# Kernel tuning notes

Hardware: AMD Instinct MI355X
Metric: run time of the kernel (lower is better)

## Reference

```python
import jax, jax.numpy as jnp
import numpy as np

N = 100000
E = 1600000
D = 128          # in_feat == hidden_size
L = 3            # hidden layers
EPS = 1e-5       # BatchNorm1d eps


def setup_inputs() -> dict:
    key = jax.random.key(0)
    ks = jax.random.split(key, 12)
    x = jax.random.normal(ks[0], (N, D), dtype=jnp.float32)
    edge_index = jax.random.randint(ks[1], (2, E), 0, N, dtype=jnp.int64)
    s = 1.0 / np.sqrt(D)
    # stacked hidden-layer SAGEConv params: lin_l (neighbor), lin_r (root), bias on lin_l
    Wl = jax.random.uniform(ks[2], (L, D, D), jnp.float32, -s, s)
    Wr = jax.random.uniform(ks[3], (L, D, D), jnp.float32, -s, s)
    b = jax.random.uniform(ks[4], (L, D), jnp.float32, -s, s)
    # batchnorm affine params
    gamma = jnp.ones((L, D), jnp.float32)
    beta = jnp.zeros((L, D), jnp.float32)
    # output SAGEConv: D -> 1
    Wl_out = jax.random.uniform(ks[5], (D, 1), jnp.float32, -s, s)
    Wr_out = jax.random.uniform(ks[6], (D, 1), jnp.float32, -s, s)
    b_out = jax.random.uniform(ks[7], (1,), jnp.float32, -s, s)
    return {"x": x, "edge_index": edge_index, "Wl": Wl, "Wr": Wr, "b": b,
            "gamma": gamma, "beta": beta, "Wl_out": Wl_out, "Wr_out": Wr_out,
            "b_out": b_out}


def _sage(x, src, dst, inv_deg, Wl, Wr, b):
    # gather neighbor features along edges, mean-aggregate at destination
    msg_sum = jax.ops.segment_sum(x[src], dst, num_segments=N)   # [N, F]
    mean = msg_sum * inv_deg                                     # 0 for isolated nodes
    return mean @ Wl + x @ Wr + b


def _batchnorm(x, gamma, beta):
    m = jnp.mean(x, axis=0)
    v = jnp.mean((x - m) ** 2, axis=0)  # biased var, as torch BN uses for normalization
    return gamma * (x - m) * jax.lax.rsqrt(v + EPS) + beta


def reference(x, edge_index, Wl, Wr, b, gamma, beta, Wl_out, Wr_out, b_out):
    src, dst = edge_index[0], edge_index[1]
    deg = jax.ops.segment_sum(jnp.ones((E,), x.dtype), dst, num_segments=N)
    inv_deg = jnp.where(deg > 0, 1.0 / jnp.maximum(deg, 1.0), 0.0)[:, None]
    h = x
    for i in range(L):
        h = _sage(h, src, dst, inv_deg, Wl[i], Wr[i], b[i])
        h = jax.nn.relu(h)
        h = _batchnorm(h, gamma[i], beta[i])
    out = _sage(h, src, dst, inv_deg, Wl_out, Wr_out, b_out)
    return jax.nn.sigmoid(out)  # [N, 1]
```

## Files before the change

### kernel.cpp

```cpp
#include <hip/hip_runtime.h>

typedef unsigned short u16;
typedef unsigned int u32;
typedef unsigned long long u64;

#define GN 100000
#define GE 1600000
#define DCAP 64
#define NRANGE 196
#define NBKT (NRANGE * 8)
#define BCAP 1536
#define LDA 136
#define CPSETS 64

typedef __bf16 bf16x8 __attribute__((ext_vector_type(8)));
typedef float f32x4 __attribute__((ext_vector_type(4)));
typedef float f32x2 __attribute__((ext_vector_type(2)));
typedef u32 u32x4 __attribute__((ext_vector_type(4)));
typedef u32 u32x2 __attribute__((ext_vector_type(2)));

__device__ __forceinline__ float bl(u32 u){ return __uint_as_float(u << 16); }
__device__ __forceinline__ float bh(u32 u){ return __uint_as_float(u & 0xffff0000u); }
__device__ __forceinline__ float bfu(u16 v){ return __uint_as_float(((u32)v) << 16); }
__device__ __forceinline__ u16 f2bf(float f){
    u32 u = __float_as_uint(f);
    u32 r = (u + 0x7fffu + ((u >> 16) & 1u)) >> 16;
    return (u16)r;
}
__device__ __forceinline__ u32 pack2(float a, float b){
    return (u32)f2bf(a) | ((u32)f2bf(b) << 16);
}
__device__ __forceinline__ u32 pk8x4(float a, float b, float c, float d){
    u32 p = (u32)__builtin_amdgcn_cvt_pk_fp8_f32(a, b, 0, false);
    p = (u32)__builtin_amdgcn_cvt_pk_fp8_f32(c, d, p, true);
    return p;
}

__global__ void __launch_bounds__(256) k_init(const int* ei, const u32* xraw,
                                              int* cursor, float* colpart, int* flags,
                                              int* bcur){
    int i = blockIdx.x * 256 + threadIdx.x;
    if (i < GN) cursor[i] = 0;
    if (i < NBKT) bcur[i] = 0;
    if (i < 3 * CPSETS * 256) colpart[i] = 0.f;
    int t = threadIdx.x;
    if (blockIdx.x == 0){
        __shared__ int s_any[4];
        int v = 0;
        #pragma unroll
        for (int j = 0; j < 4; ++j){
            int k = t * 4 + j;
            v |= ei[2 * k * 1000 + 1];
        }
        #pragma unroll
        for (int m = 1; m < 64; m <<= 1) v |= __shfl_xor(v, m);
        if ((t & 63) == 0) s_any[t >> 6] = v;
        __syncthreads();
        if (t == 0){
            int any = s_any[0] | s_any[1] | s_any[2] | s_any[3];
            flags[0] = (any == 0) ? 1 : 0;
        }
    }
    if (blockIdx.x == 1){
        __shared__ int s_cnt[4];
        int cnt = 0;
        #pragma unroll
        for (int j = 0; j < 4; ++j){
            int idx = (t * 4 + j) * 6000 + 3;
            u32 u = xraw[idx];
            int e = (u >> 7) & 0xFF;
            cnt += (e >= 100 && e <= 140) ? 1 : 0;
        }
        #pragma unroll
        for (int m = 1; m < 64; m <<= 1) cnt += __shfl_xor(cnt, m);
        if ((t & 63) == 0) s_cnt[t >> 6] = cnt;
        __syncthreads();
        if (t == 0){
            int tot = s_cnt[0] + s_cnt[1] + s_cnt[2] + s_cnt[3];
            flags[1] = (tot > 512) ? 0 : 1;
        }
    }
}

__global__ void __launch_bounds__(256) k_convx(const void* x, const int* flags,
                                               u16* xb, u32* h8){
    int tid = blockIdx.x * 256 + threadIdx.x;
    int node = tid >> 4, l15 = tid & 15;
    if (node >= GN) return;
    float f[8];
    if (flags[1]){
        const float* xf = (const float*)x + node * 128 + l15;
        #pragma unroll
        for (int a = 0; a < 8; ++a) f[a] = __builtin_nontemporal_load(xf + a * 16);
    } else {
        const u16* xh = (const u16*)x + node * 128 + l15;
        #pragma unroll
        for (int a = 0; a < 8; ++a) f[a] = bfu(xh[a * 16]);
    }
    u16* xo = xb + node * 128 + l15;
    #pragma unroll
    for (int a = 0; a < 8; ++a) xo[a * 16] = f2bf(f[a]);
    u32x2 e = { pk8x4(f[0], f[1], f[2], f[3]), pk8x4(f[4], f[5], f[6], f[7]) };
    ((u32x2*)h8)[node * 16 + l15] = e;
}

#define WOFF_WR    49152
#define WOFF_B     98304
#define WOFF_G     98688
#define WOFF_BE    99072
#define WOFF_WLO   99456
#define WOFF_WRO   99584
#define WOFF_BO    99712
#define WTOT       99713
__global__ void __launch_bounds__(256) k_convw(const void* Wl, const void* Wr, const void* b,
                                               const void* g, const void* be, const void* wlo,
                                               const void* wro, const void* bo,
                                               const int* flags, u16* wbuf, float* biasf){
    int i = blockIdx.x * 256 + threadIdx.x;
    if (i >= WTOT) return;
    const void* s; int k;
    if (i < WOFF_B){
        bool isWl = (i < WOFF_WR);
        const void* src = isWl ? Wl : Wr;
        int r = isWl ? i : i - WOFF_WR;
        int layer = r >> 14, L = r & 16383;
        int kk = isWl ? (((L & 7) << 4) | (L >> 10))
                      : (((L >> 10) << 3) | (L & 7));
        int cc = (L >> 3) & 127;
        int si = layer * 16384 + kk * 128 + cc;
        float fv = flags[1] ? ((const float*)src)[si] : bfu(((const u16*)src)[si]);
        wbuf[i] = f2bf(fv);
        return;
    }
    if      (i < WOFF_G  ){ s = b;   k = i - WOFF_B; }
    else if (i < WOFF_BE ){ s = g;   k = i - WOFF_G; }
    else if (i < WOFF_WLO){ s = be;  k = i - WOFF_BE; }
    else if (i < WOFF_WRO){ s = wlo; k = i - WOFF_WLO; }
    else if (i < WOFF_BO ){ s = wro; k = i - WOFF_WRO; }
    else                  { s = bo;  k = 0; }
    float fv = flags[1] ? ((const float*)s)[k] : bfu(((const u16*)s)[k]);
    wbuf[i] = f2bf(fv);
    if (i >= WOFF_B && i < WOFF_B + 384) biasf[i - WOFF_B] = fv;
}

__global__ void __launch_bounds__(256) k_fillA(const int* ei, const int* flags,
                                               int* bcur, u64* pairs){
    __shared__ int cnt[256];
    __shared__ int lofs[256];
    __shared__ int gbase[NRANGE];
    __shared__ int wsum[4];
    __shared__ u64 lp[1024];
    int t = threadIdx.x;
    int lane = t & 63, w = t >> 6;
    int res = blockIdx.x & 7;
    int base = blockIdx.x * 1024;
    int is64 = flags[0];
    cnt[t] = 0;
    __syncthreads();
    int myd[4], mys[4], slot[4], myr[4];
    #pragma unroll
    for (int j = 0; j < 4; ++j){
        int e = base + j * 256 + t;
        if (e < GE){
            int d, s;
            if (is64){ d = __builtin_nontemporal_load(ei + 2 * (GE + e));
                       s = __builtin_nontemporal_load(ei + 2 * e); }
            else     { d = __builtin_nontemporal_load(ei + GE + e);
                       s = __builtin_nontemporal_load(ei + e); }
            myd[j] = d; mys[j] = s; myr[j] = d >> 9;
            slot[j] = atomicAdd(&cnt[myr[j]], 1);
        } else myr[j] = -1;
    }
    __syncthreads();
    int v = cnt[t];
    int sv = v;
    #pragma unroll
    for (int d = 1; d < 64; d <<= 1){
        int u = __shfl_up(sv, d);
        if (lane >= d) sv += u;
    }
    if (lane == 63) wsum[w] = sv;
    __syncthreads();
    int prefix = 0;
    #pragma unroll
    for (int j = 0; j < 4; ++j) if (j < w) prefix += wsum[j];
    lofs[t] = sv + prefix - v;
    if (t < NRANGE && cnt[t] > 0)
        gbase[t] = atomicAdd(&bcur[t * 8 + res], cnt[t]);
    __syncthreads();
    #pragma unroll
    for (int j = 0; j < 4; ++j){
        if (myr[j] >= 0)
            lp[lofs[myr[j]] + slot[j]] = ((u64)(u32)myd[j] << 32) | (u32)mys[j];
    }
    __syncthreads();
    int total = GE - base; if (total > 1024) total = 1024;
    for (int i = t; i < total; i += 256){
        u64 pr = lp[i];
        int r = (int)(pr >> 32) >> 9;
        int g = gbase[r] + (i - lofs[r]);
        if (g < BCAP) pairs[((size_t)(r * 8 + res)) * BCAP + g] = pr;
    }
}

__global__ void __launch_bounds__(256) k_fillB(const int* bcur, const u64* pairs,
                                               int* cursor, int* col){
    int range = blockIdx.x % 200;
    int sub   = blockIdx.x / 200;
    if (range >= NRANGE || sub >= 8) return;
    int bkt = range * 8 + sub;
    int n = bcur[bkt]; if (n > BCAP) n = BCAP;
    const u64* P = pairs + (size_t)bkt * BCAP;
    for (int i = threadIdx.x; i < n; i += 256){
        u64 pr = __builtin_nontemporal_load(P + i);
        int s = (int)(u32)pr, d = (int)(pr >> 32);
        int pos = atomicAdd(&cursor[d], 1);
        if (pos < DCAP) col[d * DCAP + pos] = s;
    }
}

__global__ void __launch_bounds__(128, 6) k_gemm(const u32* h8, const int* deg, const int* col,
                                                 const u16* hin,
                                                 const u16* Wlp, const u16* Wrp,
                                                 const float* biasf, u16* hout,
                                                 u32* h8o, int write8, float* colpart){
    __shared__ u16 smA[32 * LDA];
    int t = threadIdx.x;
    int wid = t >> 6, lane = t & 63;
    int quad = lane >> 4, l15 = lane & 15;
    int r0 = blockIdx.x * 32;
    int wr0 = wid * 16;

    {
        int g8 = lane >> 3, lg8 = lane & 7;
        const u32x4* hrow4 = (const u32x4*)h8;
        #define ACC16(v) { \
            a01 += __builtin_amdgcn_cvt_pk_f32_fp8((v).x, false); \
            a23 += __builtin_amdgcn_cvt_pk_f32_fp8((v).x, true);  \
            a45 += __builtin_amdgcn_cvt_pk_f32_fp8((v).y, false); \
            a67 += __builtin_amdgcn_cvt_pk_f32_fp8((v).y, true);  \
            b01 += __builtin_amdgcn_cvt_pk_f32_fp8((v).z, false); \
            b23 += __builtin_amdgcn_cvt_pk_f32_fp8((v).z, true);  \
            b45 += __builtin_amdgcn_cvt_pk_f32_fp8((v).w, false); \
            b67 += __builtin_amdgcn_cvt_pk_f32_fp8((v).w, true); }
        #pragma unroll
        for (int m = 0; m < 2; ++m){
            int lr = wr0 + (g8 << 1) + m;
            int node = r0 + lr;
            f32x2 a01 = {0.f,0.f}, a23 = {0.f,0.f}, a45 = {0.f,0.f}, a67 = {0.f,0.f};
            f32x2 b01 = {0.f,0.f}, b23 = {0.f,0.f}, b45 = {0.f,0.f}, b67 = {0.f,0.f};
            int d = 0;
            if (node < GN){
                d = deg[node];
                int cnt = d < DCAP ? d : DCAP;
                const int* nb = col + node * DCAP;
                int e = 0;
                for (; e + 7 < cnt; e += 8){
                    int4 n0 = *(const int4*)(nb + e);
                    int4 n1 = *(const int4*)(nb + e + 4);
                    u32x4 v0 = hrow4[(size_t)n0.x * 8 + lg8];
                    u32x4 v1 = hrow4[(size_t)n0.y * 8 + lg8];
                    u32x4 v2 = hrow4[(size_t)n0.z * 8 + lg8];
                    u32x4 v3 = hrow4[(size_t)n0.w * 8 + lg8];
                    u32x4 v4 = hrow4[(size_t)n1.x * 8 + lg8];
                    u32x4 v5 = hrow4[(size_t)n1.y * 8 + lg8];
                    u32x4 v6 = hrow4[(size_t)n1.z * 8 + lg8];
                    u32x4 v7 = hrow4[(size_t)n1.w * 8 + lg8];
                    ACC16(v0) ACC16(v1) ACC16(v2) ACC16(v3)
                    ACC16(v4) ACC16(v5) ACC16(v6) ACC16(v7)
                }
                for (; e + 1 < cnt; e += 2){
                    u32x4 v0 = hrow4[(size_t)nb[e]     * 8 + lg8];
                    u32x4 v1 = hrow4[(size_t)nb[e + 1] * 8 + lg8];
                    ACC16(v0) ACC16(v1)
                }
                if (e < cnt){
                    u32x4 v0 = hrow4[(size_t)nb[e] * 8 + lg8];
                    ACC16(v0)
                }
            }
            float inv = (d > 0) ? 1.f / (float)d : 0.f;
            f32x2 iv = {inv, inv};
            a01 *= iv; a23 *= iv; a45 *= iv; a67 *= iv;
            b01 *= iv; b23 *= iv; b45 *= iv; b67 *= iv;
            u32x4 o0, o1;
            o0.x = pack2(a01.x, a01.y); o0.y = pack2(a23.x, a23.y);
            o0.z = pack2(a45.x, a45.y); o0.w = pack2(a67.x, a67.y);
            o1.x = pack2(b01.x, b01.y); o1.y = pack2(b23.x, b23.y);
            o1.z = pack2(b45.x, b45.y); o1.w = pack2(b67.x, b67.y);
            u16* wp = smA + lr * LDA + (lg8 << 4);
            *(u32x4*)wp = o0;
            *(u32x4*)(wp + 8) = o1;
        }
        #undef ACC16
    }
    __asm__ volatile("s_waitcnt lgkmcnt(0)" ::: "memory");
    __builtin_amdgcn_sched_barrier(0);

    f32x4 acc[8];
    #pragma unroll
    for (int j = 0; j < 8; j++) acc[j] = (f32x4){0.f, 0.f, 0.f, 0.f};

    int node0 = r0 + wr0 + l15;

    {
        const u32x4* Wg = (const u32x4*)Wlp;
        const u16* a0 = smA + (wr0 + l15) * LDA;
        #pragma unroll
        for (int s = 0; s < 4; ++s){
            int kc = (s << 2) + quad;
            union { u32x4 u; bf16x8 v; } fa0;
            fa0.u = *(const u32x4*)(a0 + (kc << 3));
            const u32x4* wg = Wg + (kc << 7) + l15;
            #pragma unroll
            for (int cb = 0; cb < 8; ++cb){
                union { u32x4 u; bf16x8 v; } fw;
                fw.u = wg[cb << 4];
                acc[cb] = __builtin_amdgcn_mfma_f32_16x16x32_bf16(fa0.v, fw.v, acc[cb], 0, 0, 0);
            }
        }
    }
    {
        const u32x4* Wg = (const u32x4*)Wrp;
        #pragma unroll
        for (int s = 0; s < 4; ++s){
            int kk = (s << 5) + (quad << 3);
            union { u32x4 u; bf16x8 v; } fa0;
            fa0.u = (node0 < GN) ? *(const u32x4*)(hin + node0 * 128 + kk) : (u32x4){0,0,0,0};
            int kc = (s << 2) + quad;
            const u32x4* wg = Wg + (kc << 7) + l15;
            #pragma unroll
            for (int cb = 0; cb < 8; ++cb){
                union { u32x4 u; bf16x8 v; } fw;
                fw.u = wg[cb << 4];
                acc[cb] = __builtin_amdgcn_mfma_f32_16x16x32_bf16(fa0.v, fw.v, acc[cb], 0, 0, 0);
            }
        }
    }

    float bsv[8];
    #pragma unroll
    for (int cb = 0; cb < 8; cb++) bsv[cb] = biasf[cb * 16 + l15];
    float csum[8], csq[8];
    #pragma unroll
    for (int cb = 0; cb < 8; cb++){ csum[cb] = 0.f; csq[cb] = 0.f; }

    #pragma unroll
    for (int rr = 0; rr < 4; ++rr){
        int row = r0 + wr0 + quad * 4 + rr;
        float v[8];
        #pragma unroll
        for (int cb = 0; cb < 8; ++cb) v[cb] = fmaxf(acc[cb][rr] + bsv[cb], 0.f);
        if (row < GN){
            #pragma unroll
            for (int cb = 0; cb < 8; ++cb){
                hout[row * 128 + cb * 16 + l15] = f2bf(v[cb]);
                csum[cb] += v[cb]; csq[cb] += v[cb] * v[cb];
            }
            if (write8){
                u32x2 pp = { pk8x4(v[0], v[1], v[2], v[3]),
                             pk8x4(v[4], v[5], v[6], v[7]) };
                ((u32x2*)h8o)[row * 16 + l15] = pp;
            }
        }
    }
    int base = (blockIdx.x & (CPSETS - 1)) * 256;
    #pragma unroll
    for (int cb = 0; cb < 8; cb++){
        float cs = csum[cb], cq = csq[cb];
        cs += __shfl_xor(cs, 16); cs += __shfl_xor(cs, 32);
        cq += __shfl_xor(cq, 16); cq += __shfl_xor(cq, 32);
        if (quad == 0){
            atomicAdd(&colpart[base + cb * 16 + l15], cs);
            atomicAdd(&colpart[base + 128 + cb * 16 + l15], cq);
        }
    }
}

__global__ void __launch_bounds__(256) k_bnf(const float* colpart, const u16* gamma, const u16* beta,
                                             int mode,
                                             const u16* WlN, const u16* WrN, u16* wfd,
                                             const float* bNsrc, float* bNdst,
                                             const u16* wlo, const u16* wro, const u16* bo,
                                             u16* hwl, u16* hwr, float* hb){
    __shared__ float s_sc[128], s_sh[128], s_red[256];
    int t = threadIdx.x, b = blockIdx.x;
    if (t < 128){
        float s = 0.f, q = 0.f;
        for (int j = 0; j < CPSETS; ++j){
            s += colpart[j * 256 + t];
            q += colpart[j * 256 + 128 + t];
        }
        const float invn = 1.f / (float)GN;
        float mean = s * invn;
        float var = fmaxf(q * invn - mean * mean, 0.f);
        float rstd = rsqrtf(var + 1e-5f);
        float g  = bfu(gamma[t]);
        float be = bfu(beta[t]);
        float sc = g * rstd, sh = be - mean * sc;
        s_sc[t] = sc; s_sh[t] = sh;
    }
    __syncthreads();
    if (mode == 0){
        if (b < 64){
            int idx = b * 256 + t;
            int kl = ((idx & 7) << 4) | (idx >> 10);
            int kr = ((idx >> 10) << 3) | (idx & 7);
            wfd[idx]         = f2bf(s_sc[kl] * bfu(WlN[idx]));
            wfd[16384 + idx] = f2bf(s_sc[kr] * bfu(WrN[idx]));
        } else if (t < 128){
            float acc = bNsrc[t];
            for (int k = 0; k < 128; ++k){
                int Ll = ((k & 15) << 10) + (t << 3) + (k >> 4);
                int Lr = ((k >> 3) << 10) + (t << 3) + (k & 7);
                acc += s_sh[k] * (bfu(WlN[Ll]) + bfu(WrN[Lr]));
            }
            bNdst[t] = acc;
        }
    } else if (b == 64){
        float contrib = 0.f;
        if (t < 128){
            float wl = bfu(wlo[t]), wr = bfu(wro[t]);
            hwl[t] = f2bf(s_sc[t] * wl);
            hwr[t] = f2bf(s_sc[t] * wr);
            contrib = s_sh[t] * (wl + wr);
        }
        s_red[t] = contrib;
        __syncthreads();
        for (int off = 128; off >= 1; off >>= 1){
            if (t < off) s_red[t] += s_red[t + off];
            __syncthreads();
        }
        if (t == 0) hb[0] = s_red[0] + bfu(bo[0]);
    }
}

__global__ void __launch_bounds__(256) k_dot(const u16* h, const u16* wl, const u16* wr,
                                             float* y, float* r){
    int node = (blockIdx.x * 256 + threadIdx.x) >> 6;
    int lane = threadIdx.x & 63;
    if (node >= GN) return;
    u32 hv  = ((const u32*)h)[node * 64 + lane];
    u32 wlv = ((const u32*)wl)[lane];
    u32 wrv = ((const u32*)wr)[lane];
    float hlo = bl(hv), hhi = bh(hv);
    float ya = hlo * bl(wlv) + hhi * bh(wlv);
    float ra = hlo * bl(wrv) + hhi * bh(wrv);
    #pragma unroll
    for (int m = 1; m < 64; m <<= 1){ ya += __shfl_xor(ya, m); ra += __shfl_xor(ra, m); }
    if (lane == 0){ y[node] = ya; r[node] = ra; }
}

__global__ void __launch_bounds__(64) k_out(const float* y, const float* r, const int* deg,
                                            const int* col, const float* hb,
                                            const int* flags, void* out){
    int lane = threadIdx.x;
    int grp = lane >> 4, lg = lane & 15;
    int node = blockIdx.x * 4 + grp;
    if (node >= GN) return;
    int d = deg[node];
    int cnt = d < DCAP ? d : DCAP;
    const int* nb = col + node * DCAP;
    float s = 0.f;
    for (int e = lg; e < cnt; e += 16) s += y[nb[e]];
    s += __shfl_xor(s, 1); s += __shfl_xor(s, 2);
    s += __shfl_xor(s, 4); s += __shfl_xor(s, 8);
    if (lg == 0){
        float inv = (d > 0) ? 1.f / (float)d : 0.f;
        float z = inv * s + r[node] + hb[0];
        float sg = 1.f / (1.f + __expf(-z));
        if (flags[1]) ((float*)out)[node] = sg;
        else          ((u16*)out)[node] = f2bf(sg);
    }
}

extern "C" void kernel_launch(void* const* d_in, const int* in_sizes, int n_in,
                              void* d_out, int out_size, void* d_ws, size_t ws_size,
                              hipStream_t stream) {
    const void* x     = d_in[0];
    const int*  ei    = (const int*)d_in[1];
    const void* Wl    = d_in[2];
    const void* Wr    = d_in[3];
    const void* bias  = d_in[4];
    const void* gamma = d_in[5];
    const void* beta  = d_in[6];
    const void* wlout = d_in[7];
    const void* wrout = d_in[8];
    const void* bout  = d_in[9];

    char* p = (char*)d_ws;
    auto take = [&](size_t b){ void* q = (void*)p; p += (b + 255) & ~(size_t)255; return q; };
    int*   cursor = (int*)  take((size_t)GN * 4);
    int*   flags  = (int*)  take(256);
    int*   bcur   = (int*)  take((size_t)NBKT * 4);
    float* colpart= (float*)take((size_t)3 * CPSETS * 256 * 4);
    float* biasf  = (float*)take(384 * 4);
    float* bf2    = (float*)take(128 * 4);
    float* bf3    = (float*)take(128 * 4);
    float* hb     = (float*)take(256);
    u16*   wf2    = (u16*)  take(32768 * 2);
    u16*   wf3    = (u16*)  take(32768 * 2);
    u16*   hwl    = (u16*)  take(128 * 2);
    u16*   hwr    = (u16*)  take(128 * 2);
    float* yv     = (float*)take((size_t)GN * 4);
    float* rv     = (float*)take((size_t)GN * 4);
    int*   col    = (int*)  take((size_t)GN * DCAP * 4);
    u16*   xb     = (u16*)  take((size_t)GN * 128 * 2);
    u16*   hbuf   = (u16*)  take((size_t)GN * 128 * 2);
    u32*   h8a    = (u32*)  take((size_t)GN * 128);
    u32*   h8b    = (u32*)  take((size_t)GN * 128);
    u64*   pairs  = (u64*)  take((size_t)NBKT * BCAP * 8);
    u16*   wbuf   = (u16*)  take((size_t)WTOT * 2);

    const int NB_N = (GN + 255) / 256;
    const int NB_W = (GN + 3) / 4;
    const int NB_G = (GN + 31) / 32;
    const int NB_M = (GN * 16 + 255) / 256;
    const int NB_C = (WTOT + 255) / 256;
    const int NB_A = (GE + 1023) / 1024;
    const int NB_O = (GN + 3) / 4;

    k_init <<<NB_N, 256, 0, stream>>>(ei, (const u32*)x, cursor, colpart, flags, bcur);
    k_convx<<<NB_M, 256, 0, stream>>>(x, flags, xb, h8a);
    k_convw<<<NB_C, 256, 0, stream>>>(Wl, Wr, bias, gamma, beta, wlout, wrout, bout, flags, wbuf, biasf);
    k_fillA<<<NB_A, 256, 0, stream>>>(ei, flags, bcur, pairs);
    k_fillB<<<1600, 256, 0, stream>>>(bcur, pairs, cursor, col);

    const u16* hin = xb;
    for (int i = 0; i < 3; ++i){
        const u16* Wlp; const u16* Wrp; const float* bfi;
        if (i == 0){ Wlp = wbuf;     Wrp = wbuf + WOFF_WR; bfi = biasf; }
        else if (i == 1){ Wlp = wf2; Wrp = wf2 + 16384;    bfi = bf2; }
        else { Wlp = wf3;            Wrp = wf3 + 16384;    bfi = bf3; }
        u16* wfd = (i == 0) ? wf2 : wf3;
        float* bNdst = (i == 0) ? bf2 : bf3;
        int nx = (i < 2) ? (i + 1) : 0;
        const u32* h8i = (i == 1) ? h8b : h8a;
        u32*       h8o = (i == 0) ? h8b : h8a;
        k_gemm<<<NB_G, 128, 0, stream>>>(h8i, cursor, col, hin, Wlp, Wrp, bfi,
                                         hbuf, (i == 2) ? h8b : h8o, (i < 2) ? 1 : 0,
                                         colpart + i * CPSETS * 256);
        k_bnf <<<65, 256, 0, stream>>>(colpart + i * CPSETS * 256,
            wbuf + WOFF_G + i * 128, wbuf + WOFF_BE + i * 128, (i == 2) ? 1 : 0,
            wbuf + nx * 16384, wbuf + WOFF_WR + nx * 16384, wfd,
            biasf + nx * 128, bNdst,
            wbuf + WOFF_WLO, wbuf + WOFF_WRO, wbuf + WOFF_BO, hwl, hwr, hb);
        hin = hbuf;
    }
    k_dot<<<NB_W, 256, 0, stream>>>(hbuf, hwl, hwr, yv, rv);
    k_out<<<NB_O, 64, 0, stream>>>(yv, rv, cursor, col, hb, flags, d_out);
}
```

Baseline: 433.3 us.

## Build CSR per range with shared-memory atomics and interleave two-node neighbor gathers

k_fillB now runs one block per 512-node range. It counts degrees with LDS atomics, writes the cursor directly, then scatters column indices using LDS cursors instead of global atomics. This removes global atomic traffic, but each range is now handled by a single block, which lowers parallelism. The k_gemm gather gives each lane 8 bytes of a row, so 16 lanes cover one row. Each loop iteration fetches neighbors of two nodes together to get more loads in flight, and launch bounds drop to 5 waves to leave room for the extra registers.

New measurement: 469.8 us. +8.4%, slower.

```diff
diff --git a/kernel.cpp b/kernel.cpp
--- a/kernel.cpp
+++ b/kernel.cpp
@@ -205,21 +205,46 @@
 
 __global__ void __launch_bounds__(256) k_fillB(const int* bcur, const u64* pairs,
                                                int* cursor, int* col){
-    int range = blockIdx.x % 200;
-    int sub   = blockIdx.x / 200;
-    if (range >= NRANGE || sub >= 8) return;
-    int bkt = range * 8 + sub;
-    int n = bcur[bkt]; if (n > BCAP) n = BCAP;
-    const u64* P = pairs + (size_t)bkt * BCAP;
-    for (int i = threadIdx.x; i < n; i += 256){
-        u64 pr = __builtin_nontemporal_load(P + i);
-        int s = (int)(u32)pr, d = (int)(pr >> 32);
-        int pos = atomicAdd(&cursor[d], 1);
-        if (pos < DCAP) col[d * DCAP + pos] = s;
-    }
-}
-
-__global__ void __launch_bounds__(128, 6) k_gemm(const u32* h8, const int* deg, const int* col,
+    __shared__ int cnt[512];
+    int r = blockIdx.x;
+    int t = threadIdx.x;
+    cnt[t] = 0; cnt[t + 256] = 0;
+    __syncthreads();
+    int base = r * 512;
+    int nsb[8];
+    #pragma unroll
+    for (int sb = 0; sb < 8; ++sb){
+        int n = bcur[r * 8 + sb];
+        nsb[sb] = n < BCAP ? n : BCAP;
+    }
+    #pragma unroll
+    for (int sb = 0; sb < 8; ++sb){
+        const u64* P = pairs + (size_t)(r * 8 + sb) * BCAP;
+        for (int i = t; i < nsb[sb]; i += 256){
+            int d = (int)(P[i] >> 32);
+            atomicAdd(&cnt[d - base], 1);
+        }
+    }
+    __syncthreads();
+    int n0 = base + t, n1 = base + t + 256;
+    if (n0 < GN) cursor[n0] = cnt[t];
+    if (n1 < GN) cursor[n1] = cnt[t + 256];
+    __syncthreads();
+    cnt[t] = 0; cnt[t + 256] = 0;
+    __syncthreads();
+    #pragma unroll
+    for (int sb = 0; sb < 8; ++sb){
+        const u64* P = pairs + (size_t)(r * 8 + sb) * BCAP;
+        for (int i = t; i < nsb[sb]; i += 256){
+            u64 pr = P[i];
+            int s = (int)(u32)pr, d = (int)(pr >> 32) - base;
+            int pos = atomicAdd(&cnt[d], 1);
+            if (pos < DCAP) col[(base + d) * DCAP + pos] = s;
+        }
+    }
+}
+
+__global__ void __launch_bounds__(128, 5) k_gemm(const u32* h8, const int* deg, const int* col,
                                                  const u16* hin,
                                                  const u16* Wlp, const u16* Wrp,
                                                  const float* biasf, u16* hout,
@@ -232,67 +257,90 @@
     int wr0 = wid * 16;
 
     {
-        int g8 = lane >> 3, lg8 = lane & 7;
-        const u32x4* hrow4 = (const u32x4*)h8;
-        #define ACC16(v) { \
-            a01 += __builtin_amdgcn_cvt_pk_f32_fp8((v).x, false); \
-            a23 += __builtin_amdgcn_cvt_pk_f32_fp8((v).x, true);  \
-            a45 += __builtin_amdgcn_cvt_pk_f32_fp8((v).y, false); \
-            a67 += __builtin_amdgcn_cvt_pk_f32_fp8((v).y, true);  \
-            b01 += __builtin_amdgcn_cvt_pk_f32_fp8((v).z, false); \
-            b23 += __builtin_amdgcn_cvt_pk_f32_fp8((v).z, true);  \
-            b45 += __builtin_amdgcn_cvt_pk_f32_fp8((v).w, false); \
-            b67 += __builtin_amdgcn_cvt_pk_f32_fp8((v).w, true); }
-        #pragma unroll
-        for (int m = 0; m < 2; ++m){
-            int lr = wr0 + (g8 << 1) + m;
-            int node = r0 + lr;
-            f32x2 a01 = {0.f,0.f}, a23 = {0.f,0.f}, a45 = {0.f,0.f}, a67 = {0.f,0.f};
-            f32x2 b01 = {0.f,0.f}, b23 = {0.f,0.f}, b45 = {0.f,0.f}, b67 = {0.f,0.f};
-            int d = 0;
-            if (node < GN){
-                d = deg[node];
-                int cnt = d < DCAP ? d : DCAP;
-                const int* nb = col + node * DCAP;
-                int e = 0;
-                for (; e + 7 < cnt; e += 8){
-                    int4 n0 = *(const int4*)(nb + e);
-                    int4 n1 = *(const int4*)(nb + e + 4);
-                    u32x4 v0 = hrow4[(size_t)n0.x * 8 + lg8];
-                    u32x4 v1 = hrow4[(size_t)n0.y * 8 + lg8];
-                    u32x4 v2 = hrow4[(size_t)n0.z * 8 + lg8];
-                    u32x4 v3 = hrow4[(size_t)n0.w * 8 + lg8];
-                    u32x4 v4 = hrow4[(size_t)n1.x * 8 + lg8];
-                    u32x4 v5 = hrow4[(size_t)n1.y * 8 + lg8];
-                    u32x4 v6 = hrow4[(size_t)n1.z * 8 + lg8];
-                    u32x4 v7 = hrow4[(size_t)n1.w * 8 + lg8];
-                    ACC16(v0) ACC16(v1) ACC16(v2) ACC16(v3)
-                    ACC16(v4) ACC16(v5) ACC16(v6) ACC16(v7)
-                }
-                for (; e + 1 < cnt; e += 2){
-                    u32x4 v0 = hrow4[(size_t)nb[e]     * 8 + lg8];
-                    u32x4 v1 = hrow4[(size_t)nb[e + 1] * 8 + lg8];
-                    ACC16(v0) ACC16(v1)
-                }
-                if (e < cnt){
-                    u32x4 v0 = hrow4[(size_t)nb[e] * 8 + lg8];
-                    ACC16(v0)
-                }
-            }
-            float inv = (d > 0) ? 1.f / (float)d : 0.f;
-            f32x2 iv = {inv, inv};
-            a01 *= iv; a23 *= iv; a45 *= iv; a67 *= iv;
-            b01 *= iv; b23 *= iv; b45 *= iv; b67 *= iv;
-            u32x4 o0, o1;
-            o0.x = pack2(a01.x, a01.y); o0.y = pack2(a23.x, a23.y);
-            o0.z = pack2(a45.x, a45.y); o0.w = pack2(a67.x, a67.y);
-            o1.x = pack2(b01.x, b01.y); o1.y = pack2(b23.x, b23.y);
-            o1.z = pack2(b45.x, b45.y); o1.w = pack2(b67.x, b67.y);
-            u16* wp = smA + lr * LDA + (lg8 << 4);
-            *(u32x4*)wp = o0;
-            *(u32x4*)(wp + 8) = o1;
-        }
-        #undef ACC16
+        int g16 = lane >> 4, lg = lane & 15;
+        const u32x2* hrow2 = (const u32x2*)h8;
+        #define ACC8(v, P0, P1, P2, P3) { \
+            P0 += __builtin_amdgcn_cvt_pk_f32_fp8((v).x, false); \
+            P1 += __builtin_amdgcn_cvt_pk_f32_fp8((v).x, true);  \
+            P2 += __builtin_amdgcn_cvt_pk_f32_fp8((v).y, false); \
+            P3 += __builtin_amdgcn_cvt_pk_f32_fp8((v).y, true); }
+        #pragma unroll
+        for (int pm = 0; pm < 2; ++pm){
+            int lrA = wr0 + (g16 << 2) + (pm << 1);
+            int lrB = lrA + 1;
+            int nA = r0 + lrA, nB = r0 + lrB;
+            int dA = (nA < GN) ? deg[nA] : 0;
+            int dB = (nB < GN) ? deg[nB] : 0;
+            int cA = dA < DCAP ? dA : DCAP;
+            int cB = dB < DCAP ? dB : DCAP;
+            const int* nbA = col + nA * DCAP;
+            const int* nbB = col + nB * DCAP;
+            f32x2 A0={0.f,0.f},A1={0.f,0.f},A2={0.f,0.f},A3={0.f,0.f};
+            f32x2 B0={0.f,0.f},B1={0.f,0.f},B2={0.f,0.f},B3={0.f,0.f};
+            int eA = 0, eB = 0;
+            while (eA + 7 < cA && eB + 7 < cB){
+                int4 iA0 = *(const int4*)(nbA + eA);
+                int4 iA1 = *(const int4*)(nbA + eA + 4);
+                int4 iB0 = *(const int4*)(nbB + eB);
+                int4 iB1 = *(const int4*)(nbB + eB + 4);
+                u32x2 a0 = hrow2[(size_t)iA0.x * 16 + lg];
+                u32x2 a1 = hrow2[(size_t)iA0.y * 16 + lg];
+                u32x2 a2 = hrow2[(size_t)iA0.z * 16 + lg];
+                u32x2 a3 = hrow2[(size_t)iA0.w * 16 + lg];
+                u32x2 a4 = hrow2[(size_t)iA1.x * 16 + lg];
+                u32x2 a5 = hrow2[(size_t)iA1.y * 16 + lg];
+                u32x2 a6 = hrow2[(size_t)iA1.z * 16 + lg];
+                u32x2 a7 = hrow2[(size_t)iA1.w * 16 + lg];
+                u32x2 b0 = hrow2[(size_t)iB0.x * 16 + lg];
+                u32x2 b1 = hrow2[(size_t)iB0.y * 16 + lg];
+                u32x2 b2 = hrow2[(size_t)iB0.z * 16 + lg];
+                u32x2 b3 = hrow2[(size_t)iB0.w * 16 + lg];
+                u32x2 b4 = hrow2[(size_t)iB1.x * 16 + lg];
+                u32x2 b5 = hrow2[(size_t)iB1.y * 16 + lg];
+                u32x2 b6 = hrow2[(size_t)iB1.z * 16 + lg];
+                u32x2 b7 = hrow2[(size_t)iB1.w * 16 + lg];
+                ACC8(a0,A0,A1,A2,A3) ACC8(a1,A0,A1,A2,A3)
+                ACC8(a2,A0,A1,A2,A3) ACC8(a3,A0,A1,A2,A3)
+                ACC8(a4,A0,A1,A2,A3) ACC8(a5,A0,A1,A2,A3)
+                ACC8(a6,A0,A1,A2,A3) ACC8(a7,A0,A1,A2,A3)
+                ACC8(b0,B0,B1,B2,B3) ACC8(b1,B0,B1,B2,B3)
+                ACC8(b2,B0,B1,B2,B3) ACC8(b3,B0,B1,B2,B3)
+                ACC8(b4,B0,B1,B2,B3) ACC8(b5,B0,B1,B2,B3)
+                ACC8(b6,B0,B1,B2,B3) ACC8(b7,B0,B1,B2,B3)
+                eA += 8; eB += 8;
+            }
+            for (; eA + 1 < cA; eA += 2){
+                u32x2 a0 = hrow2[(size_t)nbA[eA]     * 16 + lg];
+                u32x2 a1 = hrow2[(size_t)nbA[eA + 1] * 16 + lg];
+                ACC8(a0,A0,A1,A2,A3) ACC8(a1,A0,A1,A2,A3)
+            }
+            if (eA < cA){
+                u32x2 a0 = hrow2[(size_t)nbA[eA] * 16 + lg];
+                ACC8(a0,A0,A1,A2,A3)
+            }
+            for (; eB + 1 < cB; eB += 2){
+                u32x2 b0 = hrow2[(size_t)nbB[eB]     * 16 + lg];
+                u32x2 b1 = hrow2[(size_t)nbB[eB + 1] * 16 + lg];
+                ACC8(b0,B0,B1,B2,B3) ACC8(b1,B0,B1,B2,B3)
+            }
+            if (eB < cB){
+                u32x2 b0 = hrow2[(size_t)nbB[eB] * 16 + lg];
+                ACC8(b0,B0,B1,B2,B3)
+            }
+            float invA = (dA > 0) ? 1.f / (float)dA : 0.f;
+            float invB = (dB > 0) ? 1.f / (float)dB : 0.f;
+            f32x2 ivA = {invA, invA}, ivB = {invB, invB};
+            A0 *= ivA; A1 *= ivA; A2 *= ivA; A3 *= ivA;
+            B0 *= ivB; B1 *= ivB; B2 *= ivB; B3 *= ivB;
+            u32x4 oA, oB;
+            oA.x = pack2(A0.x, A0.y); oA.y = pack2(A1.x, A1.y);
+            oA.z = pack2(A2.x, A2.y); oA.w = pack2(A3.x, A3.y);
+            oB.x = pack2(B0.x, B0.y); oB.y = pack2(B1.x, B1.y);
+            oB.z = pack2(B2.x, B2.y); oB.w = pack2(B3.x, B3.y);
+            *(u32x4*)(smA + lrA * LDA + (lg << 3)) = oA;
+            *(u32x4*)(smA + lrB * LDA + (lg << 3)) = oB;
+        }
+        #undef ACC8
     }
     __asm__ volatile("s_waitcnt lgkmcnt(0)" ::: "memory");
     __builtin_amdgcn_sched_barrier(0);
@@ -524,7 +572,7 @@
     k_convx<<<NB_M, 256, 0, stream>>>(x, flags, xb, h8a);
     k_convw<<<NB_C, 256, 0, stream>>>(Wl, Wr, bias, gamma, beta, wlout, wrout, bout, flags, wbuf, biasf);
     k_fillA<<<NB_A, 256, 0, stream>>>(ei, flags, bcur, pairs);
-    k_fillB<<<1600, 256, 0, stream>>>(bcur, pairs, cursor, col);
+    k_fillB<<<NRANGE, 256, 0, stream>>>(bcur, pairs, cursor, col);
 
     const u16* hin = xb;
     for (int i = 0; i < 3; ++i){
```

## Build CSR columns per node range using shared-memory atomics in fillB

Applied to the files above, without the earlier changes.

The CSR fill kernel now launches one block per 512-node range instead of one per bucket. Each block first counts in-degrees with shared-memory atomics, writes them to the cursor array, then does a second pass that assigns slots with shared atomics. This replaces global atomics on the cursor array, which cuts global atomic traffic. In exchange it launches far fewer blocks (196 vs 1600), reads each range's pairs twice, and relies on cursor being written here rather than accumulated.

Result: faster. 423.0 us, median of 2 (-2.4%).

```diff
diff --git a/kernel.cpp b/kernel.cpp
--- a/kernel.cpp
+++ b/kernel.cpp
@@ -205,17 +205,42 @@
 
 __global__ void __launch_bounds__(256) k_fillB(const int* bcur, const u64* pairs,
                                                int* cursor, int* col){
-    int range = blockIdx.x % 200;
-    int sub   = blockIdx.x / 200;
-    if (range >= NRANGE || sub >= 8) return;
-    int bkt = range * 8 + sub;
-    int n = bcur[bkt]; if (n > BCAP) n = BCAP;
-    const u64* P = pairs + (size_t)bkt * BCAP;
-    for (int i = threadIdx.x; i < n; i += 256){
-        u64 pr = __builtin_nontemporal_load(P + i);
-        int s = (int)(u32)pr, d = (int)(pr >> 32);
-        int pos = atomicAdd(&cursor[d], 1);
-        if (pos < DCAP) col[d * DCAP + pos] = s;
+    __shared__ int cnt[512];
+    int r = blockIdx.x;
+    int t = threadIdx.x;
+    cnt[t] = 0; cnt[t + 256] = 0;
+    __syncthreads();
+    int base = r * 512;
+    int nsb[8];
+    #pragma unroll
+    for (int sb = 0; sb < 8; ++sb){
+        int n = bcur[r * 8 + sb];
+        nsb[sb] = n < BCAP ? n : BCAP;
+    }
+    #pragma unroll
+    for (int sb = 0; sb < 8; ++sb){
+        const u64* P = pairs + (size_t)(r * 8 + sb) * BCAP;
+        for (int i = t; i < nsb[sb]; i += 256){
+            int d = (int)(P[i] >> 32);
+            atomicAdd(&cnt[d - base], 1);
+        }
+    }
+    __syncthreads();
+    int n0 = base + t, n1 = base + t + 256;
+    if (n0 < GN) cursor[n0] = cnt[t];
+    if (n1 < GN) cursor[n1] = cnt[t + 256];
+    __syncthreads();
+    cnt[t] = 0; cnt[t + 256] = 0;
+    __syncthreads();
+    #pragma unroll
+    for (int sb = 0; sb < 8; ++sb){
+        const u64* P = pairs + (size_t)(r * 8 + sb) * BCAP;
+        for (int i = t; i < nsb[sb]; i += 256){
+            u64 pr = P[i];
+            int s = (int)(u32)pr, d = (int)(pr >> 32) - base;
+            int pos = atomicAdd(&cnt[d], 1);
+            if (pos < DCAP) col[(base + d) * DCAP + pos] = s;
+        }
     }
 }
 
@@ -524,7 +549,7 @@
     k_convx<<<NB_M, 256, 0, stream>>>(x, flags, xb, h8a);
     k_convw<<<NB_C, 256, 0, stream>>>(Wl, Wr, bias, gamma, beta, wlout, wrout, bout, flags, wbuf, biasf);
     k_fillA<<<NB_A, 256, 0, stream>>>(ei, flags, bcur, pairs);
-    k_fillB<<<1600, 256, 0, stream>>>(bcur, pairs, cursor, col);
+    k_fillB<<<NRANGE, 256, 0, stream>>>(bcur, pairs, cursor, col);
 
     const u16* hin = xb;
     for (int i = 0; i < 3; ++i){
```
